# Optimization experiments

Hardware: AMD Instinct MI355X
Metric: run time of the kernel (lower is better)

The kernel has to match this reference:

```python
import jax, jax.numpy as jnp
import numpy as np

N_NODES = 50000
N_EDGES = 600000
F_IN = 128
DIM_H = 256
N_CLASSES = 40
BN_EPS = 1e-5


def setup_inputs() -> dict:
    key = jax.random.key(0)
    ks = jax.random.split(key, 10)
    x = jax.random.normal(ks[0], (N_NODES, F_IN), dtype=jnp.float32)
    edge_index = jax.random.randint(ks[1], (2, N_EDGES), 0, N_NODES, dtype=jnp.int64)
    s1 = 1.0 / np.sqrt(F_IN)
    s2 = 1.0 / np.sqrt(DIM_H)
    W1 = jax.random.uniform(ks[2], (F_IN, DIM_H), jnp.float32, -s1, s1)
    b1 = jax.random.uniform(ks[3], (DIM_H,), jnp.float32, -s1, s1)
    gamma = jnp.ones((DIM_H,), jnp.float32)
    beta = jnp.zeros((DIM_H,), jnp.float32)
    W2 = jax.random.uniform(ks[4], (DIM_H, DIM_H), jnp.float32, -s2, s2)
    b2 = jax.random.uniform(ks[5], (DIM_H,), jnp.float32, -s2, s2)
    Wlin = jax.random.uniform(ks[6], (DIM_H, N_CLASSES), jnp.float32, -s2, s2)
    blin = jax.random.uniform(ks[7], (N_CLASSES,), jnp.float32, -s2, s2)
    return {"x": x, "edge_index": edge_index, "W1": W1, "b1": b1,
            "gamma": gamma, "beta": beta, "W2": W2, "b2": b2,
            "Wlin": Wlin, "blin": blin}


def reference(x, edge_index, W1, b1, gamma, beta, W2, b2, Wlin, blin):
    src, dst = edge_index[0], edge_index[1]
    # GIN sum aggregation: agg[i] = sum_{(j->i)} x[j]; eps = 0 (default)
    agg = jax.ops.segment_sum(x[src], dst, num_segments=N_NODES)  # [N, F_IN]
    h = x + agg
    # MLP: Linear -> BatchNorm1d (training-mode batch stats) -> ReLU -> Linear -> ReLU
    h = h @ W1 + b1                               # [N, DIM_H]
    mean = jnp.mean(h, axis=0)
    var = jnp.var(h, axis=0)                      # biased, as torch BN uses for normalization
    h = (h - mean) * jax.lax.rsqrt(var + BN_EPS) * gamma + beta
    h = jax.nn.relu(h)
    h = jax.nn.relu(h @ W2 + b2)                  # MLP final ReLU; outer x.relu() is idempotent
    return h @ Wlin + blin                        # [N, N_CLASSES]
```

## Files before the change

kernel.cpp:

```cpp
#include <hip/hip_runtime.h>

#define F_IN 128
#define DIM_H 256
#define N_CLASSES 40
#define BN_EPS 1e-5f
#define M_PAD 50176

typedef short bf16x8 __attribute__((ext_vector_type(8)));
typedef float f32x4 __attribute__((ext_vector_type(4)));

__device__ __forceinline__ unsigned short f2bf(float f) {
    union { float f; unsigned u; } v; v.f = f;
    unsigned r = v.u + 0x7fff + ((v.u >> 16) & 1);
    return (unsigned short)(r >> 16);
}
__device__ __forceinline__ float bf2f(unsigned short u) {
    union { unsigned u; float f; } v; v.u = ((unsigned)u) << 16;
    return v.f;
}
__device__ __forceinline__ float4 bf2f4(ushort4 u) {
    return make_float4(bf2f(u.x), bf2f(u.y), bf2f(u.z), bf2f(u.w));
}

__global__ void hist_kernel(const int* __restrict__ dst, int* __restrict__ hist, int nE) {
    int e = blockIdx.x * blockDim.x + threadIdx.x;
    if (e >= nE) return;
    atomicAdd(&hist[dst[e]], 1);
}

__global__ void scan_blocks_kernel(const int* __restrict__ hist,
                                   int* __restrict__ blockSums, int M) {
    __shared__ int lds[256];
    int t = threadIdx.x;
    int i = blockIdx.x * 256 + t;
    lds[t] = (i < M) ? hist[i] : 0;
    __syncthreads();
    for (int off = 128; off > 0; off >>= 1) {
        if (t < off) lds[t] += lds[t + off];
        __syncthreads();
    }
    if (t == 0) blockSums[blockIdx.x] = lds[0];
}

__global__ void scan_final_kernel(const int* __restrict__ hist,
                                  const int* __restrict__ blockSums,
                                  int* __restrict__ start, int M, int nE) {
    __shared__ int lds[256];
    int t = threadIdx.x;
    lds[t] = (t < blockIdx.x) ? blockSums[t] : 0;
    __syncthreads();
    for (int o = 128; o > 0; o >>= 1) {
        if (t < o) lds[t] += lds[t + o];
        __syncthreads();
    }
    int off = lds[0];
    __syncthreads();
    int i = blockIdx.x * 256 + t;
    int orig = (i < M) ? hist[i] : 0;
    lds[t] = orig;
    __syncthreads();
    for (int o = 1; o < 256; o <<= 1) {
        int v = (t >= o) ? lds[t - o] : 0;
        __syncthreads();
        lds[t] += v;
        __syncthreads();
    }
    if (i < M) start[i] = off + lds[t] - orig;
    if (blockIdx.x == 0 && t == 0) start[M] = nE;
}

__global__ void fill_kernel(const int* __restrict__ src, const int* __restrict__ dst,
                            const int* __restrict__ start, int* __restrict__ cursor,
                            int* __restrict__ order, int nE) {
    int e = blockIdx.x * blockDim.x + threadIdx.x;
    if (e >= nE) return;
    int d = dst[e];
    int pos = start[d] + atomicAdd(&cursor[d], 1);
    order[pos] = src[e];
}

__global__ void prep_kernel(const float* __restrict__ x, unsigned short* __restrict__ xb,
                            const float* __restrict__ W1, const float* __restrict__ W2,
                            const float* __restrict__ Wl,
                            unsigned short* __restrict__ W1t,
                            unsigned short* __restrict__ W2t,
                            unsigned short* __restrict__ Wlt,
                            int* __restrict__ histz,
                            int XQ, int ZQ) {
    int idx = blockIdx.x * 256 + threadIdx.x;
    if (idx < XQ) {
        float4 v = ((const float4*)x)[idx];
        ushort4 o;
        o.x = f2bf(v.x); o.y = f2bf(v.y); o.z = f2bf(v.z); o.w = f2bf(v.w);
        ((ushort4*)xb)[idx] = o;
        return;
    }
    int j = idx - XQ;
    if (j < 32768) {
        int n = j >> 7, k = j & 127;
        W1t[j] = f2bf(W1[k * DIM_H + n]);
    } else if (j < 32768 + 65536) {
        int i = j - 32768;
        int n = i >> 8, k = i & 255;
        W2t[i] = f2bf(W2[k * DIM_H + n]);
    } else if (j < 32768 + 65536 + 16384) {
        int i = j - 98304;
        int n = i >> 8, k = i & 255;
        Wlt[i] = f2bf((n < N_CLASSES) ? Wl[k * N_CLASSES + n] : 0.f);
    } else {
        int z = j - 114688;
        if (z >= 0 && z < ZQ) ((int4*)histz)[z] = make_int4(0, 0, 0, 0);
    }
}

__global__ void bn_reduce_kernel(const float* __restrict__ partials, int R,
                                 const float* __restrict__ gamma,
                                 const float* __restrict__ beta,
                                 float* __restrict__ scale,
                                 float* __restrict__ shift, int M) {
    __shared__ float ls[256], lss[256];
    int c = blockIdx.x, t = threadIdx.x;
    float s = 0.f, ss = 0.f;
    for (int r = t; r < R; r += 256) {
        s += partials[(long)r * 512 + c];
        ss += partials[(long)r * 512 + 256 + c];
    }
    ls[t] = s; lss[t] = ss;
    __syncthreads();
    for (int o = 128; o > 0; o >>= 1) {
        if (t < o) { ls[t] += ls[t + o]; lss[t] += lss[t + o]; }
        __syncthreads();
    }
    if (t == 0) {
        float inv = 1.0f / (float)M;
        float mean = ls[0] * inv;
        float var = lss[0] * inv - mean * mean;
        float sc = gamma[c] * rsqrtf(var + BN_EPS);
        scale[c] = sc;
        shift[c] = beta[c] - mean * sc;
    }
}

__global__ __launch_bounds__(256, 4) void gin_gemm1_kernel(
    const unsigned short* __restrict__ xb,
    const int* __restrict__ order, const int* __restrict__ start,
    const unsigned short* __restrict__ W1t, const float* __restrict__ b1,
    unsigned short* __restrict__ h1, float* __restrict__ partials, int M) {
    constexpr int K = F_IN, S = K / 32;
    constexpr int PA = 136;
    constexpr int PB = 40;
    constexpr int PH = 264;
    __shared__ __align__(16) unsigned short lds[64 * PA + 256 * PB];
    unsigned short* At = lds;
    unsigned short* Bs = lds + 64 * PA;
    unsigned short* h1t = lds;

    int tid = threadIdx.x;
    int wave = tid >> 6, lane = tid & 63;
    int l15 = lane & 15, q = lane >> 4;
    int wn = wave;
    long row0 = (long)blockIdx.x * 64;

    bf16x8 br[4];
    auto loadB = [&](int s) {
#pragma unroll
        for (int i = 0; i < 4; ++i) {
            int ch = tid + i * 256;
            int m = ch >> 2, c = ch & 3;
            br[i] = *(const bf16x8*)(W1t + m * K + s * 32 + c * 8);
        }
    };
    auto writeB = [&]() {
#pragma unroll
        for (int i = 0; i < 4; ++i) {
            int ch = tid + i * 256;
            int m = ch >> 2, c = ch & 3;
            *(bf16x8*)(&Bs[m * PB + c * 8]) = br[i];
        }
    };

    loadB(0);

    {
        int hw = tid >> 5, lane32 = tid & 31;
        const ushort4* xv = (const ushort4*)xb;
        for (int rr = 0; rr < 8; ++rr) {
            int r = rr * 8 + hw;
            long node = row0 + r;
            float4 a0 = make_float4(0.f, 0.f, 0.f, 0.f);
            float4 a1 = a0, a2 = a0, a3 = a0;
            if (node < M) {
                a0 = bf2f4(xv[node * 32 + lane32]);
                int e0 = start[node], e1 = start[node + 1];
                int e = e0;
                for (; e + 8 <= e1; e += 8) {
                    int s0 = order[e],     s1 = order[e + 1], s2 = order[e + 2], s3 = order[e + 3];
                    int s4 = order[e + 4], s5 = order[e + 5], s6 = order[e + 6], s7 = order[e + 7];
                    ushort4 u0 = xv[(size_t)s0 * 32 + lane32];
                    ushort4 u1 = xv[(size_t)s1 * 32 + lane32];
                    ushort4 u2 = xv[(size_t)s2 * 32 + lane32];
                    ushort4 u3 = xv[(size_t)s3 * 32 + lane32];
                    ushort4 u4 = xv[(size_t)s4 * 32 + lane32];
                    ushort4 u5 = xv[(size_t)s5 * 32 + lane32];
                    ushort4 u6 = xv[(size_t)s6 * 32 + lane32];
                    ushort4 u7 = xv[(size_t)s7 * 32 + lane32];
                    float4 v0 = bf2f4(u0), v1 = bf2f4(u1), v2 = bf2f4(u2), v3 = bf2f4(u3);
                    float4 v4 = bf2f4(u4), v5 = bf2f4(u5), v6 = bf2f4(u6), v7 = bf2f4(u7);
                    a0.x += v0.x; a0.y += v0.y; a0.z += v0.z; a0.w += v0.w;
                    a1.x += v1.x; a1.y += v1.y; a1.z += v1.z; a1.w += v1.w;
                    a2.x += v2.x; a2.y += v2.y; a2.z += v2.z; a2.w += v2.w;
                    a3.x += v3.x; a3.y += v3.y; a3.z += v3.z; a3.w += v3.w;
                    a0.x += v4.x; a0.y += v4.y; a0.z += v4.z; a0.w += v4.w;
                    a1.x += v5.x; a1.y += v5.y; a1.z += v5.z; a1.w += v5.w;
                    a2.x += v6.x; a2.y += v6.y; a2.z += v6.z; a2.w += v6.w;
                    a3.x += v7.x; a3.y += v7.y; a3.z += v7.z; a3.w += v7.w;
                }
                for (; e + 4 <= e1; e += 4) {
                    int s0 = order[e], s1 = order[e + 1], s2 = order[e + 2], s3 = order[e + 3];
                    float4 v0 = bf2f4(xv[(size_t)s0 * 32 + lane32]);
                    float4 v1 = bf2f4(xv[(size_t)s1 * 32 + lane32]);
                    float4 v2 = bf2f4(xv[(size_t)s2 * 32 + lane32]);
                    float4 v3 = bf2f4(xv[(size_t)s3 * 32 + lane32]);
                    a0.x += v0.x; a0.y += v0.y; a0.z += v0.z; a0.w += v0.w;
                    a1.x += v1.x; a1.y += v1.y; a1.z += v1.z; a1.w += v1.w;
                    a2.x += v2.x; a2.y += v2.y; a2.z += v2.z; a2.w += v2.w;
                    a3.x += v3.x; a3.y += v3.y; a3.z += v3.z; a3.w += v3.w;
                }
                for (; e < e1; ++e) {
                    float4 v = bf2f4(xv[(size_t)order[e] * 32 + lane32]);
                    a1.x += v.x; a1.y += v.y; a1.z += v.z; a1.w += v.w;
                }
            }
            float4 t;
            t.x = (a0.x + a1.x) + (a2.x + a3.x);
            t.y = (a0.y + a1.y) + (a2.y + a3.y);
            t.z = (a0.z + a1.z) + (a2.z + a3.z);
            t.w = (a0.w + a1.w) + (a2.w + a3.w);
            ushort4 o;
            o.x = f2bf(t.x); o.y = f2bf(t.y); o.z = f2bf(t.z); o.w = f2bf(t.w);
            *(ushort4*)(&At[r * PA + lane32 * 4]) = o;
        }
    }
    writeB();
    __syncthreads();

    f32x4 acc[4][4] = {};
#pragma unroll
    for (int s = 0; s < S; ++s) {
        if (s + 1 < S) loadB(s + 1);
        bf16x8 af[4], bfr[4];
#pragma unroll
        for (int mt = 0; mt < 4; ++mt)
            af[mt] = *(const bf16x8*)(&At[(mt * 16 + l15) * PA + s * 32 + q * 8]);
#pragma unroll
        for (int nt = 0; nt < 4; ++nt)
            bfr[nt] = *(const bf16x8*)(&Bs[(wn * 64 + nt * 16 + l15) * PB + q * 8]);
#pragma unroll
        for (int mt = 0; mt < 4; ++mt)
#pragma unroll
            for (int nt = 0; nt < 4; ++nt)
                acc[mt][nt] = __builtin_amdgcn_mfma_f32_16x16x32_bf16(
                    af[mt], bfr[nt], acc[mt][nt], 0, 0, 0);
        __syncthreads();
        if (s + 1 < S) { writeB(); __syncthreads(); }
    }

#pragma unroll
    for (int nt = 0; nt < 4; ++nt) {
        int col = wn * 64 + nt * 16 + l15;
        float b = b1[col];
        float s = 0.f, ss = 0.f;
#pragma unroll
        for (int mt = 0; mt < 4; ++mt) {
#pragma unroll
            for (int r = 0; r < 4; ++r) {
                long row = row0 + mt * 16 + q * 4 + r;
                float v = acc[mt][nt][r] + b;
                if (row < M) { s += v; ss += v * v; }
                h1t[(mt * 16 + q * 4 + r) * PH + col] = f2bf(v);
            }
        }
        s += __shfl_xor(s, 16, 64);  s += __shfl_xor(s, 32, 64);
        ss += __shfl_xor(ss, 16, 64); ss += __shfl_xor(ss, 32, 64);
        if (lane < 16) {
            partials[(long)blockIdx.x * 512 + col] = s;
            partials[(long)blockIdx.x * 512 + 256 + col] = ss;
        }
    }
    __syncthreads();
    {
        int srow = tid >> 2, scol = (tid & 3) * 64;
        unsigned short* dst = h1 + (row0 + srow) * DIM_H + scol;
        const unsigned short* srcp = &h1t[srow * PH + scol];
#pragma unroll
        for (int j = 0; j < 8; ++j)
            *(bf16x8*)(dst + j * 8) = *(const bf16x8*)(srcp + j * 8);
    }
}

__global__ __launch_bounds__(512, 4) void gemm23_kernel(
    const unsigned short* __restrict__ h1, const unsigned short* __restrict__ W2t,
    const float* __restrict__ b2,
    const float* __restrict__ scale, const float* __restrict__ shift,
    const unsigned short* __restrict__ Wlt, const float* __restrict__ blin,
    float* __restrict__ out, int M) {
    constexpr int S = 8;
    constexpr int PA = 40, PB = 40, PH = 264;
    constexpr int STAGE = 128 * PA + 256 * PB;
    __shared__ __align__(16) unsigned short lds[128 * PH];
    unsigned short* h2t = lds;

    int tid = threadIdx.x;
    int wave = tid >> 6, lane = tid & 63;
    int wm = wave >> 2, wn = wave & 3;
    int l15 = lane & 15, q = lane >> 4;
    long row0 = (long)blockIdx.x * 128;

    int am = tid >> 2, ac = tid & 3;
    bf16x8 ar, br[2];
    auto loadAB = [&](int s) {
        ar = *(const bf16x8*)(h1 + (row0 + am) * DIM_H + s * 32 + ac * 8);
#pragma unroll
        for (int i = 0; i < 2; ++i) {
            int ch = tid + i * 512;
            int m = ch >> 2, c = ch & 3;
            br[i] = *(const bf16x8*)(W2t + m * DIM_H + s * 32 + c * 8);
        }
    };
    auto writeAB = [&](int s, int buf) {
        unsigned short* As = lds + buf * STAGE;
        unsigned short* Bs = As + 128 * PA;
        {
            int kb = s * 32 + ac * 8;
            float4 sc0 = *(const float4*)(scale + kb);
            float4 sc1 = *(const float4*)(scale + kb + 4);
            float4 sh0 = *(const float4*)(shift + kb);
            float4 sh1 = *(const float4*)(shift + kb + 4);
            float scv[8] = {sc0.x, sc0.y, sc0.z, sc0.w, sc1.x, sc1.y, sc1.z, sc1.w};
            float shv[8] = {sh0.x, sh0.y, sh0.z, sh0.w, sh1.x, sh1.y, sh1.z, sh1.w};
            bf16x8 v = ar;
#pragma unroll
            for (int j = 0; j < 8; ++j) {
                float f = bf2f((unsigned short)v[j]);
                f = fmaxf(f * scv[j] + shv[j], 0.f);
                v[j] = (short)f2bf(f);
            }
            *(bf16x8*)(&As[am * PA + ac * 8]) = v;
        }
#pragma unroll
        for (int i = 0; i < 2; ++i) {
            int ch = tid + i * 512;
            int m = ch >> 2, c = ch & 3;
            *(bf16x8*)(&Bs[m * PB + c * 8]) = br[i];
        }
    };

    f32x4 acc[4][4] = {};
    loadAB(0);
    writeAB(0, 0);
#pragma unroll
    for (int s = 0; s < S; ++s) {
        if (s + 1 < S) loadAB(s + 1);
        __syncthreads();
        const unsigned short* As = lds + (s & 1) * STAGE;
        const unsigned short* Bs = As + 128 * PA;
        bf16x8 af[4], bfr[4];
#pragma unroll
        for (int mt = 0; mt < 4; ++mt)
            af[mt] = *(const bf16x8*)(&As[(wm * 64 + mt * 16 + l15) * PA + q * 8]);
#pragma unroll
        for (int nt = 0; nt < 4; ++nt)
            bfr[nt] = *(const bf16x8*)(&Bs[(wn * 64 + nt * 16 + l15) * PB + q * 8]);
#pragma unroll
        for (int mt = 0; mt < 4; ++mt)
#pragma unroll
            for (int nt = 0; nt < 4; ++nt)
                acc[mt][nt] = __builtin_amdgcn_mfma_f32_16x16x32_bf16(
                    af[mt], bfr[nt], acc[mt][nt], 0, 0, 0);
        if (s + 1 < S) writeAB(s + 1, (s + 1) & 1);
    }
    __syncthreads();

#pragma unroll
    for (int nt = 0; nt < 4; ++nt) {
        int colL = wn * 64 + nt * 16 + l15;
        float b = b2[colL];
#pragma unroll
        for (int mt = 0; mt < 4; ++mt)
#pragma unroll
            for (int r = 0; r < 4; ++r) {
                int rowL = wm * 64 + mt * 16 + q * 4 + r;
                h2t[rowL * PH + colL] = f2bf(fmaxf(acc[mt][nt][r] + b, 0.f));
            }
    }
    __syncthreads();

    f32x4 acc3[3] = {};
#pragma unroll
    for (int s = 0; s < 8; ++s) {
        bf16x8 a3 = *(const bf16x8*)(&h2t[(wave * 16 + l15) * PH + s * 32 + q * 8]);
#pragma unroll
        for (int nt = 0; nt < 3; ++nt) {
            bf16x8 b3 = *(const bf16x8*)(Wlt + (nt * 16 + l15) * 256 + s * 32 + q * 8);
            acc3[nt] = __builtin_amdgcn_mfma_f32_16x16x32_bf16(a3, b3, acc3[nt], 0, 0, 0);
        }
    }
#pragma unroll
    for (int nt = 0; nt < 3; ++nt) {
        int col = nt * 16 + l15;
        if (col < N_CLASSES) {
            float b = blin[col];
#pragma unroll
            for (int r = 0; r < 4; ++r) {
                long row = row0 + wave * 16 + q * 4 + r;
                if (row < M) out[row * N_CLASSES + col] = acc3[nt][r] + b;
            }
        }
    }
}

extern "C" void kernel_launch(void* const* d_in, const int* in_sizes, int n_in,
                              void* d_out, int out_size, void* d_ws, size_t ws_size,
                              hipStream_t stream) {
    const float* x     = (const float*)d_in[0];
    const int*   ei    = (const int*)d_in[1];
    const float* W1    = (const float*)d_in[2];
    const float* b1    = (const float*)d_in[3];
    const float* gamma = (const float*)d_in[4];
    const float* beta  = (const float*)d_in[5];
    const float* W2    = (const float*)d_in[6];
    const float* b2    = (const float*)d_in[7];
    const float* Wlin  = (const float*)d_in[8];
    const float* blin  = (const float*)d_in[9];
    float* out = (float*)d_out;

    int M  = in_sizes[0] / F_IN;
    int nE = in_sizes[1] / 2;
    const int* srcIdx = ei;
    const int* dstIdx = ei + nE;
    int nB = (M + 255) / 256;
    int gy1 = (M + 63) / 64;
    int gy23 = (M + 127) / 128;
    int XQ = M * 32;
    int ZQ = 2 * M / 4;

    unsigned short* h1bf  = (unsigned short*)d_ws;
    unsigned short* xb    = h1bf + (size_t)M_PAD * DIM_H;
    unsigned short* W1t   = xb + (size_t)M_PAD * F_IN;
    unsigned short* W2t   = W1t + DIM_H * F_IN;
    unsigned short* Wlt   = W2t + DIM_H * DIM_H;
    float*          partials = (float*)(Wlt + 64 * DIM_H);
    float*          scale = partials + (size_t)800 * 512;
    float*          shift = scale + DIM_H;
    int*            hist  = (int*)(shift + DIM_H);
    int*            cursor= hist + M;
    int*            start = cursor + M;
    int*            blockSums = start + (M + 1);
    int*            order = blockSums + 256;

    int tB = 256;
    prep_kernel<<<(XQ + 114688 + ZQ + 255) / 256, 256, 0, stream>>>(
        x, xb, W1, W2, Wlin, W1t, W2t, Wlt, hist, XQ, ZQ);
    hist_kernel<<<(nE + tB - 1) / tB, tB, 0, stream>>>(dstIdx, hist, nE);
    scan_blocks_kernel<<<nB, 256, 0, stream>>>(hist, blockSums, M);
    scan_final_kernel<<<nB, 256, 0, stream>>>(hist, blockSums, start, M, nE);
    fill_kernel<<<(nE + tB - 1) / tB, tB, 0, stream>>>(srcIdx, dstIdx, start, cursor, order, nE);

    gin_gemm1_kernel<<<gy1, 256, 0, stream>>>(xb, order, start, W1t, b1, h1bf, partials, M);
    bn_reduce_kernel<<<DIM_H, 256, 0, stream>>>(partials, gy1, gamma, beta, scale, shift, M);
    gemm23_kernel<<<gy23, 512, 0, stream>>>(h1bf, W2t, b2, scale, shift, Wlt, blin, out, M);
}
```

Before: 239.7 us.

## Split gather from GEMM1 and use 128-row double-buffered GEMM1 tiles

The fused gather+GEMM1 kernel is split into a standalone neighbor-gather kernel that writes the aggregated bf16 rows to a workspace buffer, plus a separate GEMM1 kernel. The new GEMM1 uses 512 threads, 128-row tiles and double-buffered LDS stages for both A and B, with partial BN stats written per half-tile. The aim is to decouple latency-bound irregular gathers from MFMA work so each kernel gets better occupancy. The cost is an extra round trip of the aggregated matrix through global memory and one more launch.

Measured after the change: 233.4 us. -2.6%, faster.

```diff
diff --git a/kernel.cpp b/kernel.cpp
--- a/kernel.cpp
+++ b/kernel.cpp
@@ -85,8 +85,7 @@
                             unsigned short* __restrict__ W1t,
                             unsigned short* __restrict__ W2t,
                             unsigned short* __restrict__ Wlt,
-                            int* __restrict__ histz,
-                            int XQ, int ZQ) {
+                            int* __restrict__ histz, int XQ, int ZQ) {
     int idx = blockIdx.x * 256 + threadIdx.x;
     if (idx < XQ) {
         float4 v = ((const float4*)x)[idx];
@@ -141,117 +140,118 @@
     }
 }
 
-__global__ __launch_bounds__(256, 4) void gin_gemm1_kernel(
+__global__ __launch_bounds__(256) void gather_kernel(
     const unsigned short* __restrict__ xb,
     const int* __restrict__ order, const int* __restrict__ start,
-    const unsigned short* __restrict__ W1t, const float* __restrict__ b1,
-    unsigned short* __restrict__ h1, float* __restrict__ partials, int M) {
-    constexpr int K = F_IN, S = K / 32;
-    constexpr int PA = 136;
-    constexpr int PB = 40;
-    constexpr int PH = 264;
-    __shared__ __align__(16) unsigned short lds[64 * PA + 256 * PB];
-    unsigned short* At = lds;
-    unsigned short* Bs = lds + 64 * PA;
+    unsigned short* __restrict__ A1, int M) {
+    int node = blockIdx.x * 8 + (threadIdx.x >> 5);
+    if (node >= M) return;
+    int lane32 = threadIdx.x & 31;
+    const ushort4* xv = (const ushort4*)xb;
+    float4 a0 = bf2f4(xv[(size_t)node * 32 + lane32]);
+    float4 a1 = make_float4(0.f, 0.f, 0.f, 0.f);
+    float4 a2 = a1, a3 = a1;
+    int e0 = start[node], e1 = start[node + 1];
+    int e = e0;
+    for (; e + 8 <= e1; e += 8) {
+        int s0 = order[e],     s1 = order[e + 1], s2 = order[e + 2], s3 = order[e + 3];
+        int s4 = order[e + 4], s5 = order[e + 5], s6 = order[e + 6], s7 = order[e + 7];
+        ushort4 u0 = xv[(size_t)s0 * 32 + lane32];
+        ushort4 u1 = xv[(size_t)s1 * 32 + lane32];
+        ushort4 u2 = xv[(size_t)s2 * 32 + lane32];
+        ushort4 u3 = xv[(size_t)s3 * 32 + lane32];
+        ushort4 u4 = xv[(size_t)s4 * 32 + lane32];
+        ushort4 u5 = xv[(size_t)s5 * 32 + lane32];
+        ushort4 u6 = xv[(size_t)s6 * 32 + lane32];
+        ushort4 u7 = xv[(size_t)s7 * 32 + lane32];
+        float4 v0 = bf2f4(u0), v1 = bf2f4(u1), v2 = bf2f4(u2), v3 = bf2f4(u3);
+        float4 v4 = bf2f4(u4), v5 = bf2f4(u5), v6 = bf2f4(u6), v7 = bf2f4(u7);
+        a0.x += v0.x; a0.y += v0.y; a0.z += v0.z; a0.w += v0.w;
+        a1.x += v1.x; a1.y += v1.y; a1.z += v1.z; a1.w += v1.w;
+        a2.x += v2.x; a2.y += v2.y; a2.z += v2.z; a2.w += v2.w;
+        a3.x += v3.x; a3.y += v3.y; a3.z += v3.z; a3.w += v3.w;
+        a0.x += v4.x; a0.y += v4.y; a0.z += v4.z; a0.w += v4.w;
+        a1.x += v5.x; a1.y += v5.y; a1.z += v5.z; a1.w += v5.w;
+        a2.x += v6.x; a2.y += v6.y; a2.z += v6.z; a2.w += v6.w;
+        a3.x += v7.x; a3.y += v7.y; a3.z += v7.z; a3.w += v7.w;
+    }
+    for (; e + 4 <= e1; e += 4) {
+        int s0 = order[e], s1 = order[e + 1], s2 = order[e + 2], s3 = order[e + 3];
+        float4 v0 = bf2f4(xv[(size_t)s0 * 32 + lane32]);
+        float4 v1 = bf2f4(xv[(size_t)s1 * 32 + lane32]);
+        float4 v2 = bf2f4(xv[(size_t)s2 * 32 + lane32]);
+        float4 v3 = bf2f4(xv[(size_t)s3 * 32 + lane32]);
+        a0.x += v0.x; a0.y += v0.y; a0.z += v0.z; a0.w += v0.w;
+        a1.x += v1.x; a1.y += v1.y; a1.z += v1.z; a1.w += v1.w;
+        a2.x += v2.x; a2.y += v2.y; a2.z += v2.z; a2.w += v2.w;
+        a3.x += v3.x; a3.y += v3.y; a3.z += v3.z; a3.w += v3.w;
+    }
+    for (; e < e1; ++e) {
+        float4 v = bf2f4(xv[(size_t)order[e] * 32 + lane32]);
+        a1.x += v.x; a1.y += v.y; a1.z += v.z; a1.w += v.w;
+    }
+    float4 t;
+    t.x = (a0.x + a1.x) + (a2.x + a3.x);
+    t.y = (a0.y + a1.y) + (a2.y + a3.y);
+    t.z = (a0.z + a1.z) + (a2.z + a3.z);
+    t.w = (a0.w + a1.w) + (a2.w + a3.w);
+    ushort4 o;
+    o.x = f2bf(t.x); o.y = f2bf(t.y); o.z = f2bf(t.z); o.w = f2bf(t.w);
+    ((ushort4*)A1)[(size_t)node * 32 + lane32] = o;
+}
+
+__global__ __launch_bounds__(512, 4) void gemm1_kernel(
+    const unsigned short* __restrict__ A1, const unsigned short* __restrict__ W1t,
+    const float* __restrict__ b1, unsigned short* __restrict__ h1,
+    float* __restrict__ partials, int M) {
+    constexpr int S = 4;
+    constexpr int PA = 40, PB = 40, PH = 264;
+    constexpr int STAGE = 128 * PA + 256 * PB;
+    __shared__ __align__(16) unsigned short lds[128 * PH];
     unsigned short* h1t = lds;
 
     int tid = threadIdx.x;
     int wave = tid >> 6, lane = tid & 63;
+    int wm = wave >> 2, wn = wave & 3;
     int l15 = lane & 15, q = lane >> 4;
-    int wn = wave;
-    long row0 = (long)blockIdx.x * 64;
-
-    bf16x8 br[4];
-    auto loadB = [&](int s) {
-#pragma unroll
-        for (int i = 0; i < 4; ++i) {
-            int ch = tid + i * 256;
+    long row0 = (long)blockIdx.x * 128;
+
+    int am = tid >> 2, ac = tid & 3;
+    bf16x8 ar, br[2];
+    auto loadAB = [&](int s) {
+        ar = *(const bf16x8*)(A1 + (row0 + am) * F_IN + s * 32 + ac * 8);
+#pragma unroll
+        for (int i = 0; i < 2; ++i) {
+            int ch = tid + i * 512;
             int m = ch >> 2, c = ch & 3;
-            br[i] = *(const bf16x8*)(W1t + m * K + s * 32 + c * 8);
+            br[i] = *(const bf16x8*)(W1t + m * F_IN + s * 32 + c * 8);
         }
     };
-    auto writeB = [&]() {
-#pragma unroll
-        for (int i = 0; i < 4; ++i) {
-            int ch = tid + i * 256;
+    auto writeAB = [&](int buf) {
+        unsigned short* As = lds + buf * STAGE;
+        unsigned short* Bs = As + 128 * PA;
+        *(bf16x8*)(&As[am * PA + ac * 8]) = ar;
+#pragma unroll
+        for (int i = 0; i < 2; ++i) {
+            int ch = tid + i * 512;
             int m = ch >> 2, c = ch & 3;
             *(bf16x8*)(&Bs[m * PB + c * 8]) = br[i];
         }
     };
 
-    loadB(0);
-
-    {
-        int hw = tid >> 5, lane32 = tid & 31;
-        const ushort4* xv = (const ushort4*)xb;
-        for (int rr = 0; rr < 8; ++rr) {
-            int r = rr * 8 + hw;
-            long node = row0 + r;
-            float4 a0 = make_float4(0.f, 0.f, 0.f, 0.f);
-            float4 a1 = a0, a2 = a0, a3 = a0;
-            if (node < M) {
-                a0 = bf2f4(xv[node * 32 + lane32]);
-                int e0 = start[node], e1 = start[node + 1];
-                int e = e0;
-                for (; e + 8 <= e1; e += 8) {
-                    int s0 = order[e],     s1 = order[e + 1], s2 = order[e + 2], s3 = order[e + 3];
-                    int s4 = order[e + 4], s5 = order[e + 5], s6 = order[e + 6], s7 = order[e + 7];
-                    ushort4 u0 = xv[(size_t)s0 * 32 + lane32];
-                    ushort4 u1 = xv[(size_t)s1 * 32 + lane32];
-                    ushort4 u2 = xv[(size_t)s2 * 32 + lane32];
-                    ushort4 u3 = xv[(size_t)s3 * 32 + lane32];
-                    ushort4 u4 = xv[(size_t)s4 * 32 + lane32];
-                    ushort4 u5 = xv[(size_t)s5 * 32 + lane32];
-                    ushort4 u6 = xv[(size_t)s6 * 32 + lane32];
-                    ushort4 u7 = xv[(size_t)s7 * 32 + lane32];
-                    float4 v0 = bf2f4(u0), v1 = bf2f4(u1), v2 = bf2f4(u2), v3 = bf2f4(u3);
-                    float4 v4 = bf2f4(u4), v5 = bf2f4(u5), v6 = bf2f4(u6), v7 = bf2f4(u7);
-                    a0.x += v0.x; a0.y += v0.y; a0.z += v0.z; a0.w += v0.w;
-                    a1.x += v1.x; a1.y += v1.y; a1.z += v1.z; a1.w += v1.w;
-                    a2.x += v2.x; a2.y += v2.y; a2.z += v2.z; a2.w += v2.w;
-                    a3.x += v3.x; a3.y += v3.y; a3.z += v3.z; a3.w += v3.w;
-                    a0.x += v4.x; a0.y += v4.y; a0.z += v4.z; a0.w += v4.w;
-                    a1.x += v5.x; a1.y += v5.y; a1.z += v5.z; a1.w += v5.w;
-                    a2.x += v6.x; a2.y += v6.y; a2.z += v6.z; a2.w += v6.w;
-                    a3.x += v7.x; a3.y += v7.y; a3.z += v7.z; a3.w += v7.w;
-                }
-                for (; e + 4 <= e1; e += 4) {
-                    int s0 = order[e], s1 = order[e + 1], s2 = order[e + 2], s3 = order[e + 3];
-                    float4 v0 = bf2f4(xv[(size_t)s0 * 32 + lane32]);
-                    float4 v1 = bf2f4(xv[(size_t)s1 * 32 + lane32]);
-                    float4 v2 = bf2f4(xv[(size_t)s2 * 32 + lane32]);
-                    float4 v3 = bf2f4(xv[(size_t)s3 * 32 + lane32]);
-                    a0.x += v0.x; a0.y += v0.y; a0.z += v0.z; a0.w += v0.w;
-                    a1.x += v1.x; a1.y += v1.y; a1.z += v1.z; a1.w += v1.w;
-                    a2.x += v2.x; a2.y += v2.y; a2.z += v2.z; a2.w += v2.w;
-                    a3.x += v3.x; a3.y += v3.y; a3.z += v3.z; a3.w += v3.w;
-                }
-                for (; e < e1; ++e) {
-                    float4 v = bf2f4(xv[(size_t)order[e] * 32 + lane32]);
-                    a1.x += v.x; a1.y += v.y; a1.z += v.z; a1.w += v.w;
-                }
-            }
-            float4 t;
-            t.x = (a0.x + a1.x) + (a2.x + a3.x);
-            t.y = (a0.y + a1.y) + (a2.y + a3.y);
-            t.z = (a0.z + a1.z) + (a2.z + a3.z);
-            t.w = (a0.w + a1.w) + (a2.w + a3.w);
-            ushort4 o;
-            o.x = f2bf(t.x); o.y = f2bf(t.y); o.z = f2bf(t.z); o.w = f2bf(t.w);
-            *(ushort4*)(&At[r * PA + lane32 * 4]) = o;
-        }
-    }
-    writeB();
-    __syncthreads();
-
     f32x4 acc[4][4] = {};
+    loadAB(0);
+    writeAB(0);
 #pragma unroll
     for (int s = 0; s < S; ++s) {
-        if (s + 1 < S) loadB(s + 1);
+        if (s + 1 < S) loadAB(s + 1);
+        __syncthreads();
+        const unsigned short* As = lds + (s & 1) * STAGE;
+        const unsigned short* Bs = As + 128 * PA;
         bf16x8 af[4], bfr[4];
 #pragma unroll
         for (int mt = 0; mt < 4; ++mt)
-            af[mt] = *(const bf16x8*)(&At[(mt * 16 + l15) * PA + s * 32 + q * 8]);
+            af[mt] = *(const bf16x8*)(&As[(wm * 64 + mt * 16 + l15) * PA + q * 8]);
 #pragma unroll
         for (int nt = 0; nt < 4; ++nt)
             bfr[nt] = *(const bf16x8*)(&Bs[(wn * 64 + nt * 16 + l15) * PB + q * 8]);
@@ -261,9 +261,9 @@
             for (int nt = 0; nt < 4; ++nt)
                 acc[mt][nt] = __builtin_amdgcn_mfma_f32_16x16x32_bf16(
                     af[mt], bfr[nt], acc[mt][nt], 0, 0, 0);
-        __syncthreads();
-        if (s + 1 < S) { writeB(); __syncthreads(); }
-    }
+        if (s + 1 < S) writeAB((s + 1) & 1);
+    }
+    __syncthreads();
 
 #pragma unroll
     for (int nt = 0; nt < 4; ++nt) {
@@ -274,17 +274,18 @@
         for (int mt = 0; mt < 4; ++mt) {
 #pragma unroll
             for (int r = 0; r < 4; ++r) {
-                long row = row0 + mt * 16 + q * 4 + r;
+                long row = row0 + wm * 64 + mt * 16 + q * 4 + r;
                 float v = acc[mt][nt][r] + b;
                 if (row < M) { s += v; ss += v * v; }
-                h1t[(mt * 16 + q * 4 + r) * PH + col] = f2bf(v);
+                h1t[(wm * 64 + mt * 16 + q * 4 + r) * PH + col] = f2bf(v);
             }
         }
         s += __shfl_xor(s, 16, 64);  s += __shfl_xor(s, 32, 64);
         ss += __shfl_xor(ss, 16, 64); ss += __shfl_xor(ss, 32, 64);
         if (lane < 16) {
-            partials[(long)blockIdx.x * 512 + col] = s;
-            partials[(long)blockIdx.x * 512 + 256 + col] = ss;
+            long pr = (long)blockIdx.x * 2 + wm;
+            partials[pr * 512 + col] = s;
+            partials[pr * 512 + 256 + col] = ss;
         }
     }
     __syncthreads();
@@ -439,14 +440,14 @@
     const int* srcIdx = ei;
     const int* dstIdx = ei + nE;
     int nB = (M + 255) / 256;
-    int gy1 = (M + 63) / 64;
-    int gy23 = (M + 127) / 128;
+    int g128 = (M + 127) / 128;
     int XQ = M * 32;
     int ZQ = 2 * M / 4;
 
     unsigned short* h1bf  = (unsigned short*)d_ws;
     unsigned short* xb    = h1bf + (size_t)M_PAD * DIM_H;
-    unsigned short* W1t   = xb + (size_t)M_PAD * F_IN;
+    unsigned short* A1bf  = xb + (size_t)M_PAD * F_IN;
+    unsigned short* W1t   = A1bf + (size_t)M_PAD * F_IN;
     unsigned short* W2t   = W1t + DIM_H * F_IN;
     unsigned short* Wlt   = W2t + DIM_H * DIM_H;
     float*          partials = (float*)(Wlt + 64 * DIM_H);
@@ -466,7 +467,8 @@
     scan_final_kernel<<<nB, 256, 0, stream>>>(hist, blockSums, start, M, nE);
     fill_kernel<<<(nE + tB - 1) / tB, tB, 0, stream>>>(srcIdx, dstIdx, start, cursor, order, nE);
 
-    gin_gemm1_kernel<<<gy1, 256, 0, stream>>>(xb, order, start, W1t, b1, h1bf, partials, M);
-    bn_reduce_kernel<<<DIM_H, 256, 0, stream>>>(partials, gy1, gamma, beta, scale, shift, M);
-    gemm23_kernel<<<gy23, 512, 0, stream>>>(h1bf, W2t, b2, scale, shift, Wlt, blin, out, M);
-}
+    gather_kernel<<<(M + 7) / 8, 256, 0, stream>>>(xb, order, start, A1bf, M);
+    gemm1_kernel<<<g128, 512, 0, stream>>>(A1bf, W1t, b1, h1bf, partials, M);
+    bn_reduce_kernel<<<DIM_H, 256, 0, stream>>>(partials, 2 * g128, gamma, beta, scale, shift, M);
+    gemm23_kernel<<<g128, 512, 0, stream>>>(h1bf, W2t, b2, scale, shift, Wlt, blin, out, M);
+}
```
